# Kernel optimization log

Measured on AMD Instinct MI355X. Metric: run time of the kernel, lower is better.

## Reference

```python
import jax, jax.numpy as jnp
import numpy as np

BLANK = 36
NEG = -1e30  # stand-in for -inf that stays NaN-free under logaddexp


def _ctc_loss(logits, targets, input_lengths, target_lengths):
    """CTC loss (reduction='mean', matching torch.nn.CTCLoss semantics:
    per-sample loss divided by target_length, then mean over batch).
    logits: [B, T, C] raw scores; targets: [B*L] flattened labels (fixed L per sample).
    """
    B, T, C = logits.shape
    L = targets.shape[0] // B
    tgt = targets.reshape(B, L)
    S = 2 * L + 1  # extended label length: blank-interleaved

    # log_softmax over classes, then time-major [T, B, C]
    lp = jnp.transpose(jax.nn.log_softmax(logits, axis=-1), (1, 0, 2))

    # extended targets: [blank, t1, blank, t2, ..., blank]  -> [B, S]
    ext = jnp.full((B, S), BLANK, dtype=tgt.dtype).at[:, 1::2].set(tgt)

    # gather log-probs of extended labels: [T, B, S]
    lp_ext = lp[:, jnp.arange(B)[:, None], ext]

    # positions beyond 2*target_len are invalid
    valid = jnp.arange(S)[None, :] < (2 * target_lengths[:, None] + 1)  # [B, S]
    # skip transition s-2 -> s allowed only if ext[s] != blank and ext[s] != ext[s-2]
    skip_ok = (ext != BLANK) & jnp.concatenate(
        [jnp.zeros((B, 2), bool), ext[:, 2:] != ext[:, :-2]], axis=1)

    end_idx = 2 * target_lengths  # index of final blank; [B]

    def final_ll(alpha):
        e1 = jnp.take_along_axis(alpha, end_idx[:, None], axis=1)[:, 0]
        e2 = jnp.take_along_axis(alpha, (end_idx - 1)[:, None], axis=1)[:, 0]
        return jnp.logaddexp(e1, e2)

    # t = 0 initialization
    alpha0 = jnp.full((B, S), NEG, logits.dtype)
    alpha0 = alpha0.at[:, 0].set(lp_ext[0, :, 0]).at[:, 1].set(lp_ext[0, :, 1])
    alpha0 = jnp.where(valid, alpha0, NEG)
    final0 = jnp.where(input_lengths == 1, final_ll(alpha0), NEG)

    pad1 = jnp.full((B, 1), NEG, logits.dtype)
    pad2 = jnp.full((B, 2), NEG, logits.dtype)

    def step(carry, inp):
        alpha, final = carry
        t, lpe = inp  # lpe: [B, S]
        a1 = jnp.concatenate([pad1, alpha[:, :-1]], axis=1)
        a2 = jnp.where(skip_ok, jnp.concatenate([pad2, alpha[:, :-2]], axis=1), NEG)
        new = jnp.logaddexp(jnp.logaddexp(alpha, a1), a2) + lpe
        new = jnp.where(valid, new, NEG)
        final = jnp.where(input_lengths == t + 1, final_ll(new), final)
        return (new, final), None

    (_, final), _ = jax.lax.scan(step, (alpha0, final0),
                                 (jnp.arange(1, T), lp_ext[1:]))
    return jnp.mean(-final / target_lengths.astype(logits.dtype))


def setup_inputs() -> dict:
    key = jax.random.key(0)
    k1, k2 = jax.random.split(key)
    B, T, C, L = 2048, 256, 37, 16
    logits = jax.random.normal(k1, (B, T, C), dtype=jnp.float32)
    targets = jax.random.randint(k2, (B * L,), 0, 36, dtype=jnp.int32)  # never blank
    input_lengths = jnp.full((B,), T, dtype=jnp.int32)
    target_lengths = jnp.full((B,), L, dtype=jnp.int32)
    return {"logits": logits, "targets": targets,
            "input_lengths": input_lengths, "target_lengths": target_lengths}


def reference(logits, targets, input_lengths, target_lengths):
    return _ctc_loss(logits, targets, input_lengths, target_lengths)
```

## Files before the change

### kernel.cpp

```cpp
#include <hip/hip_runtime.h>

#define BLANK 36
#define NEG -1e30f
#define CC 37

__device__ __forceinline__ float logaddexp_f(float a, float b) {
    float m = fmaxf(a, b);
    float d = fabsf(a - b);
    return m + __logf(1.0f + __expf(-d));
}

__global__ __launch_bounds__(256) void ctc_fused_kernel(
    const float* __restrict__ logits,
    const int*   __restrict__ targets,
    const int*   __restrict__ input_lengths,
    const int*   __restrict__ target_lengths,
    float*       __restrict__ per_sample,
    int B, int T, int L)
{
    __shared__ float lds[4 * 4992];
    const int lane = threadIdx.x & 63;
    const int wib  = threadIdx.x >> 6;
    const int b    = blockIdx.x * 4 + wib;
    if (b >= B) return;

    float* X0 = lds + wib * 4992;
    float* X1 = X0 + 2368;
    float* D0 = X0 + 4736;
    float* D1 = D0 + 64;

    const int S = 2 * L + 1;
    const int tlen = target_lengths[b];
    const int ilen = input_lengths[b];
    const int end_idx = 2 * tlen;

    int ext_s = BLANK;
    if (lane < S && (lane & 1)) ext_s = targets[b * L + (lane >> 1)];
    const int ext_sm2 = __shfl_up(ext_s, 2);
    const bool skip_ok = (lane < S) && (lane >= 2) && (ext_s != BLANK) && (ext_s != ext_sm2);
    const bool valid = lane < (2 * tlen + 1);

    const float4* src = (const float4*)(logits + (size_t)b * T * CC);

    float alpha = NEG, cap = NEG;

    auto STEP = [&](float lpe, int tt) {
        float a1 = __shfl_up(alpha, 1);
        a1 = (lane == 0) ? NEG : a1;
        float a2 = __shfl_up(alpha, 2);
        a2 = skip_ok ? a2 : NEG;
        const float mm = fmaxf(fmaxf(alpha, a1), a2);
        const float ss = __expf(alpha - mm) + __expf(a1 - mm) + __expf(a2 - mm);
        alpha = valid ? (mm + __logf(ss) + lpe) : NEG;
        cap = (ilen == tt + 1) ? alpha : cap;
    };

    {
        float4* dst = (float4*)X0;
        #pragma unroll
        for (int k = 0; k < 9; ++k) dst[k * 64 + lane] = src[k * 64 + lane];
        if (lane < 16) dst[576 + lane] = src[576 + lane];
        __builtin_amdgcn_s_waitcnt(0);
        const float* xr = X0 + lane * CC;
        float m = xr[0];
        #pragma unroll
        for (int c2 = 1; c2 < CC; ++c2) m = fmaxf(m, xr[c2]);
        float ss = 0.0f;
        #pragma unroll
        for (int c2 = 0; c2 < CC; ++c2) ss += __expf(xr[c2] - m);
        D0[lane] = m + __logf(ss);
        __builtin_amdgcn_s_waitcnt(0);
    }

    const int NC = T >> 6;
    for (int c = 0; c < NC; ++c) {
        float* Xb = (c & 1) ? X1 : X0;
        float* Db = (c & 1) ? D1 : D0;
        const bool more = (c + 1 < NC);

        float4 f0 = {}, f1 = {}, f2 = {}, f3 = {}, f4 = {},
               f5 = {}, f6 = {}, f7 = {}, f8 = {}, f9 = {};
        if (more) {
            const float4* s2 = src + (size_t)(c + 1) * 592;
            f0 = s2[lane];       f1 = s2[64 + lane];  f2 = s2[128 + lane];
            f3 = s2[192 + lane]; f4 = s2[256 + lane]; f5 = s2[320 + lane];
            f6 = s2[384 + lane]; f7 = s2[448 + lane]; f8 = s2[512 + lane];
            if (lane < 16) f9 = s2[576 + lane];
        }

        const int tbase = c << 6;
        float p0 = Xb[0 * CC + ext_s] - Db[0];
        float p1 = Xb[1 * CC + ext_s] - Db[1];
        float p2 = Xb[2 * CC + ext_s] - Db[2];
        float p3 = Xb[3 * CC + ext_s] - Db[3];
        float q0, q1, q2, q3;
        int g = 0;
        if (c == 0) {
            alpha = (valid && lane <= 1) ? p0 : NEG;
            cap = (ilen == 1) ? alpha : cap;
            q0 = Xb[4 * CC + ext_s] - Db[4];
            q1 = Xb[5 * CC + ext_s] - Db[5];
            q2 = Xb[6 * CC + ext_s] - Db[6];
            q3 = Xb[7 * CC + ext_s] - Db[7];
            STEP(p1, 1); STEP(p2, 2); STEP(p3, 3);
            p0 = q0; p1 = q1; p2 = q2; p3 = q3;
            g = 1;
        }
        for (; g < 16; ++g) {
            const int r = (g + 1) << 2;
            if (g < 15) {
                q0 = Xb[(r + 0) * CC + ext_s] - Db[r + 0];
                q1 = Xb[(r + 1) * CC + ext_s] - Db[r + 1];
                q2 = Xb[(r + 2) * CC + ext_s] - Db[r + 2];
                q3 = Xb[(r + 3) * CC + ext_s] - Db[r + 3];
            }
            const int tt = tbase + (g << 2);
            STEP(p0, tt); STEP(p1, tt + 1); STEP(p2, tt + 2); STEP(p3, tt + 3);
            p0 = q0; p1 = q1; p2 = q2; p3 = q3;
        }

        if (more) {
            float* Xn = (c & 1) ? X0 : X1;
            float* Dn = (c & 1) ? D0 : D1;
            float4* dst = (float4*)Xn;
            dst[lane] = f0;       dst[64 + lane] = f1;  dst[128 + lane] = f2;
            dst[192 + lane] = f3; dst[256 + lane] = f4; dst[320 + lane] = f5;
            dst[384 + lane] = f6; dst[448 + lane] = f7; dst[512 + lane] = f8;
            if (lane < 16) dst[576 + lane] = f9;
            __builtin_amdgcn_s_waitcnt(0);
            const float* xr = Xn + lane * CC;
            float m = xr[0];
            #pragma unroll
            for (int c2 = 1; c2 < CC; ++c2) m = fmaxf(m, xr[c2]);
            float ss = 0.0f;
            #pragma unroll
            for (int c2 = 0; c2 < CC; ++c2) ss += __expf(xr[c2] - m);
            Dn[lane] = m + __logf(ss);
            __builtin_amdgcn_s_waitcnt(0);
        }
    }

    const float e1 = __shfl(cap, end_idx);
    const float e2 = __shfl(cap, end_idx - 1);
    const float final_v = logaddexp_f(e1, e2);
    if (lane == 0) per_sample[b] = -final_v / (float)tlen;
}

__global__ __launch_bounds__(256) void lse_kernel(
    const float* __restrict__ logits, float* __restrict__ denom, int N)
{
    __shared__ float lds[256 * CC];
    const int lane = threadIdx.x & 63;
    const int wib  = threadIdx.x >> 6;
    const int wave = blockIdx.x * 4 + wib;
    const long long row0 = (long long)wave * 64;
    if (row0 >= N) return;
    const int wbase = wib * 64 * CC;
    const float4* src4 = (const float4*)(logits + row0 * CC);
    const long long n4_remaining = ((long long)N * CC - row0 * CC) / 4;
    float4* lds4 = (float4*)(lds + wbase);
    #pragma unroll
    for (int k = 0; k < 10; ++k) {
        const int idx = k * 64 + lane;
        if (idx < 592 && idx < n4_remaining) lds4[idx] = src4[idx];
    }
    __builtin_amdgcn_s_waitcnt(0);
    const long long row = row0 + lane;
    if (row >= N) return;
    const float* x = lds + wbase + lane * CC;
    float m = x[0];
    #pragma unroll
    for (int c = 1; c < CC; ++c) m = fmaxf(m, x[c]);
    float s = 0.0f;
    #pragma unroll
    for (int c = 0; c < CC; ++c) s += __expf(x[c] - m);
    denom[row] = m + __logf(s);
}

__global__ __launch_bounds__(256) void ctc_alpha2_kernel(
    const float* __restrict__ logits, const float* __restrict__ denom,
    const int* __restrict__ targets, const int* __restrict__ input_lengths,
    const int* __restrict__ target_lengths, float* __restrict__ per_sample,
    int B, int T, int L)
{
    const int wave = (int)((blockIdx.x * blockDim.x + threadIdx.x) >> 6);
    const int lane = threadIdx.x & 63;
    if (wave >= B) return;
    const int b = wave;
    const int S = 2 * L + 1;
    const int tlen = target_lengths[b];
    const int ilen = input_lengths[b];
    const int end_idx = 2 * tlen;
    int ext_s = BLANK;
    if (lane < S && (lane & 1)) ext_s = targets[b * L + (lane >> 1)];
    const int ext_sm2 = __shfl_up(ext_s, 2);
    const bool skip_ok = (lane < S) && (lane >= 2) && (ext_s != BLANK) && (ext_s != ext_sm2);
    const bool valid = lane < (2 * tlen + 1);
    const float* lg = logits + (size_t)b * T * CC;
    const float* dn = denom + (size_t)b * T;
    float x_cur = lg[ext_s];
    float d_cur = dn[0];
    float x_nx = (T > 1) ? lg[CC + ext_s] : 0.0f;
    float d_nx = (T > 1) ? dn[1] : 0.0f;
    float final_v = NEG;
    float alpha = (valid && lane <= 1) ? (x_cur - d_cur) : NEG;
    if (ilen == 1) {
        const float e1 = __shfl(alpha, end_idx);
        const float e2 = __shfl(alpha, end_idx - 1);
        final_v = logaddexp_f(e1, e2);
    }
    for (int tt = 1; tt < T; ++tt) {
        x_cur = x_nx; d_cur = d_nx;
        if (tt + 1 < T) {
            x_nx = lg[(size_t)(tt + 1) * CC + ext_s];
            d_nx = dn[tt + 1];
        }
        const float lpe = x_cur - d_cur;
        float a1 = __shfl_up(alpha, 1);
        if (lane == 0) a1 = NEG;
        float a2 = __shfl_up(alpha, 2);
        if (!skip_ok) a2 = NEG;
        const float m = fmaxf(fmaxf(alpha, a1), a2);
        const float s = __expf(alpha - m) + __expf(a1 - m) + __expf(a2 - m);
        const float na = m + __logf(s) + lpe;
        alpha = valid ? na : NEG;
        if (ilen == tt + 1) {
            const float e1 = __shfl(alpha, end_idx);
            const float e2 = __shfl(alpha, end_idx - 1);
            final_v = logaddexp_f(e1, e2);
        }
    }
    if (lane == 0) per_sample[b] = -final_v / (float)tlen;
}

__global__ __launch_bounds__(256) void ctc_alpha_mono_kernel(
    const float* __restrict__ logits, const int* __restrict__ targets,
    const int* __restrict__ input_lengths, const int* __restrict__ target_lengths,
    float* __restrict__ per_sample, int B, int T, int L)
{
    const int wave = (int)((blockIdx.x * blockDim.x + threadIdx.x) >> 6);
    const int lane = threadIdx.x & 63;
    if (wave >= B) return;
    const int b = wave;
    const int S = 2 * L + 1;
    const int tlen = target_lengths[b];
    const int ilen = input_lengths[b];
    const int end_idx = 2 * tlen;
    int ext_s = BLANK;
    if (lane < S && (lane & 1)) ext_s = targets[b * L + (lane >> 1)];
    const int ext_sm2 = __shfl_up(ext_s, 2);
    const bool skip_ok = (lane < S) && (lane >= 2) && (ext_s != BLANK) && (ext_s != ext_sm2);
    const bool valid = lane < (2 * tlen + 1);
    const float* lg = logits + (size_t)b * T * CC;
    float alpha = NEG, final_v = NEG;
    for (int t = 0; t < T; ++t) {
        float x = (lane < CC) ? lg[t * CC + lane] : -3.0e38f;
        float mx = x;
        #pragma unroll
        for (int o = 32; o > 0; o >>= 1) mx = fmaxf(mx, __shfl_xor(mx, o));
        float e = (lane < CC) ? __expf(x - mx) : 0.0f;
        float se = e;
        #pragma unroll
        for (int o = 32; o > 0; o >>= 1) se += __shfl_xor(se, o);
        const float lp = x - mx - __logf(se);
        const float lpe = __shfl(lp, ext_s);
        float newa;
        if (t == 0) {
            newa = (lane <= 1) ? lpe : NEG;
        } else {
            float a1 = __shfl_up(alpha, 1);
            if (lane == 0) a1 = NEG;
            float a2 = __shfl_up(alpha, 2);
            if (!skip_ok) a2 = NEG;
            newa = logaddexp_f(logaddexp_f(alpha, a1), a2) + lpe;
        }
        if (!valid) newa = NEG;
        alpha = newa;
        if (ilen == t + 1) {
            const float e1 = __shfl(alpha, end_idx);
            const float e2 = __shfl(alpha, end_idx - 1);
            final_v = logaddexp_f(e1, e2);
        }
    }
    if (lane == 0) per_sample[b] = -final_v / (float)tlen;
}

__global__ __launch_bounds__(256) void reduce_mean_kernel(
    const float* __restrict__ ps, float* __restrict__ out, int B)
{
    float s = 0.0f;
    for (int i = threadIdx.x; i < B; i += 256) s += ps[i];
    #pragma unroll
    for (int o = 32; o > 0; o >>= 1) s += __shfl_xor(s, o);
    __shared__ float sm[4];
    const int w = threadIdx.x >> 6, l = threadIdx.x & 63;
    if (l == 0) sm[w] = s;
    __syncthreads();
    if (threadIdx.x == 0) {
        out[0] = (sm[0] + sm[1] + sm[2] + sm[3]) / (float)B;
    }
}

extern "C" void kernel_launch(void* const* d_in, const int* in_sizes, int n_in,
                              void* d_out, int out_size, void* d_ws, size_t ws_size,
                              hipStream_t stream) {
    const float* logits         = (const float*)d_in[0];
    const int*   targets        = (const int*)d_in[1];
    const int*   input_lengths  = (const int*)d_in[2];
    const int*   target_lengths = (const int*)d_in[3];

    const int B = in_sizes[2];
    const int L = in_sizes[1] / B;
    const int T = in_sizes[0] / (B * CC);
    const long long N = (long long)B * T;

    float* per_sample = (float*)d_ws;
    float* scratch    = per_sample + B;
    float* out        = (float*)d_out;

    const size_t ws_mid = ((size_t)B + (size_t)N) * sizeof(float);
    const int nblocks_alpha = (B * 64 + 255) / 256;
    const long long nwaves = (N + 63) / 64;

    if ((T % 64 == 0) && T >= 64 && L <= 31 && ws_size >= (size_t)B * sizeof(float)) {
        ctc_fused_kernel<<<(B + 3) / 4, 256, 0, stream>>>(
            logits, targets, input_lengths, target_lengths, per_sample, B, T, L);
    } else if (ws_size >= ws_mid && T >= 2) {
        lse_kernel<<<(int)((nwaves + 3) / 4), 256, 0, stream>>>(logits, scratch, (int)N);
        ctc_alpha2_kernel<<<nblocks_alpha, 256, 0, stream>>>(
            logits, scratch, targets, input_lengths, target_lengths, per_sample, B, T, L);
    } else {
        ctc_alpha_mono_kernel<<<nblocks_alpha, 256, 0, stream>>>(
            logits, targets, input_lengths, target_lengths, per_sample, B, T, L);
    }
    reduce_mean_kernel<<<1, 256, 0, stream>>>(per_sample, out, B);
}
```

Baseline: 144.7 us.

## Run CTC forward recursion in scaled linear space instead of log space

```diff
diff --git a/kernel.cpp b/kernel.cpp
--- a/kernel.cpp
+++ b/kernel.cpp
@@ -3,6 +3,7 @@
 #define BLANK 36
 #define NEG -1e30f
 #define CC 37
+#define LOG32 3.4657359027997265f
 
 __device__ __forceinline__ float logaddexp_f(float a, float b) {
     float m = fmaxf(a, b);
@@ -10,7 +11,7 @@
     return m + __logf(1.0f + __expf(-d));
 }
 
-__global__ __launch_bounds__(256) void ctc_fused_kernel(
+__global__ __launch_bounds__(256) void ctc_fused_lin_kernel(
     const float* __restrict__ logits,
     const int*   __restrict__ targets,
     const int*   __restrict__ input_lengths,
@@ -18,41 +19,68 @@
     float*       __restrict__ per_sample,
     int B, int T, int L)
 {
-    __shared__ float lds[4 * 4992];
+    __shared__ float lds[4 * 4736];
     const int lane = threadIdx.x & 63;
     const int wib  = threadIdx.x >> 6;
     const int b    = blockIdx.x * 4 + wib;
     if (b >= B) return;
 
-    float* X0 = lds + wib * 4992;
+    float* X0 = lds + wib * 4736;
     float* X1 = X0 + 2368;
-    float* D0 = X0 + 4736;
-    float* D1 = D0 + 64;
 
     const int S = 2 * L + 1;
-    const int tlen = target_lengths[b];
-    const int ilen = input_lengths[b];
-    const int end_idx = 2 * tlen;
+    const int tlen_s = __builtin_amdgcn_readfirstlane(target_lengths[b]);
+    const int ilen_s = __builtin_amdgcn_readfirstlane(input_lengths[b]);
+    const int end_s  = 2 * tlen_s;
 
     int ext_s = BLANK;
     if (lane < S && (lane & 1)) ext_s = targets[b * L + (lane >> 1)];
     const int ext_sm2 = __shfl_up(ext_s, 2);
     const bool skip_ok = (lane < S) && (lane >= 2) && (ext_s != BLANK) && (ext_s != ext_sm2);
-    const bool valid = lane < (2 * tlen + 1);
+    const bool valid = lane < (2 * tlen_s + 1);
 
     const float4* src = (const float4*)(logits + (size_t)b * T * CC);
 
-    float alpha = NEG, cap = NEG;
-
-    auto STEP = [&](float lpe, int tt) {
-        float a1 = __shfl_up(alpha, 1);
-        a1 = (lane == 0) ? NEG : a1;
-        float a2 = __shfl_up(alpha, 2);
-        a2 = skip_ok ? a2 : NEG;
-        const float mm = fmaxf(fmaxf(alpha, a1), a2);
-        const float ss = __expf(alpha - mm) + __expf(a1 - mm) + __expf(a2 - mm);
-        alpha = valid ? (mm + __logf(ss) + lpe) : NEG;
-        cap = (ilen == tt + 1) ? alpha : cap;
+    float z    = 0.0f;
+    float racc = 0.0f;
+    float capv = NEG;
+
+    auto ZSTEP = [&](float p, int tt) {
+        float z1 = __shfl_up(z, 1);
+        z1 = (lane == 0) ? 0.0f : z1;
+        float z2 = __shfl_up(z, 2);
+        z2 = skip_ok ? z2 : 0.0f;
+        const float zn = (z + z1 + z2) * p;
+        z = valid ? zn : 0.0f;
+        if (ilen_s == tt + 1) {
+            capv = __logf(fmaxf(z, 1e-35f)) + racc - (float)(tt + 1) * LOG32;
+        }
+    };
+
+    auto RESCALE = [&]() {
+        float m = z;
+        #pragma unroll
+        for (int o = 32; o > 0; o >>= 1) m = fmaxf(m, __shfl_xor(m, o));
+        m = fmaxf(m, 1e-30f);
+        z *= (1.0f / m);
+        racc += __logf(m);
+    };
+
+    auto SOFTMAX = [&](float* Xn) {
+        float xr[CC];
+        const float* row = Xn + lane * CC;
+        #pragma unroll
+        for (int c2 = 0; c2 < CC; ++c2) xr[c2] = row[c2];
+        float m = xr[0];
+        #pragma unroll
+        for (int c2 = 1; c2 < CC; ++c2) m = fmaxf(m, xr[c2]);
+        float ss = 0.0f;
+        #pragma unroll
+        for (int c2 = 0; c2 < CC; ++c2) { xr[c2] = __expf(xr[c2] - m); ss += xr[c2]; }
+        const float inv = 32.0f / ss;
+        float* wrow = Xn + lane * CC;
+        #pragma unroll
+        for (int c2 = 0; c2 < CC; ++c2) wrow[c2] = xr[c2] * inv;
     };
 
     {
@@ -61,21 +89,13 @@
         for (int k = 0; k < 9; ++k) dst[k * 64 + lane] = src[k * 64 + lane];
         if (lane < 16) dst[576 + lane] = src[576 + lane];
         __builtin_amdgcn_s_waitcnt(0);
-        const float* xr = X0 + lane * CC;
-        float m = xr[0];
-        #pragma unroll
-        for (int c2 = 1; c2 < CC; ++c2) m = fmaxf(m, xr[c2]);
-        float ss = 0.0f;
-        #pragma unroll
-        for (int c2 = 0; c2 < CC; ++c2) ss += __expf(xr[c2] - m);
-        D0[lane] = m + __logf(ss);
+        SOFTMAX(X0);
         __builtin_amdgcn_s_waitcnt(0);
     }
 
     const int NC = T >> 6;
     for (int c = 0; c < NC; ++c) {
         float* Xb = (c & 1) ? X1 : X0;
-        float* Db = (c & 1) ? D1 : D0;
         const bool more = (c + 1 < NC);
 
         float4 f0 = {}, f1 = {}, f2 = {}, f3 = {}, f4 = {},
@@ -89,61 +109,54 @@
         }
 
         const int tbase = c << 6;
-        float p0 = Xb[0 * CC + ext_s] - Db[0];
-        float p1 = Xb[1 * CC + ext_s] - Db[1];
-        float p2 = Xb[2 * CC + ext_s] - Db[2];
-        float p3 = Xb[3 * CC + ext_s] - Db[3];
+        float p0 = Xb[0 * CC + ext_s];
+        float p1 = Xb[1 * CC + ext_s];
+        float p2 = Xb[2 * CC + ext_s];
+        float p3 = Xb[3 * CC + ext_s];
         float q0, q1, q2, q3;
         int g = 0;
         if (c == 0) {
-            alpha = (valid && lane <= 1) ? p0 : NEG;
-            cap = (ilen == 1) ? alpha : cap;
-            q0 = Xb[4 * CC + ext_s] - Db[4];
-            q1 = Xb[5 * CC + ext_s] - Db[5];
-            q2 = Xb[6 * CC + ext_s] - Db[6];
-            q3 = Xb[7 * CC + ext_s] - Db[7];
-            STEP(p1, 1); STEP(p2, 2); STEP(p3, 3);
+            z = (valid && lane <= 1) ? p0 : 0.0f;
+            if (ilen_s == 1) capv = __logf(fmaxf(z, 1e-35f)) - LOG32;
+            q0 = Xb[4 * CC + ext_s];
+            q1 = Xb[5 * CC + ext_s];
+            q2 = Xb[6 * CC + ext_s];
+            q3 = Xb[7 * CC + ext_s];
+            ZSTEP(p1, 1); ZSTEP(p2, 2); ZSTEP(p3, 3);
             p0 = q0; p1 = q1; p2 = q2; p3 = q3;
             g = 1;
         }
         for (; g < 16; ++g) {
             const int r = (g + 1) << 2;
             if (g < 15) {
-                q0 = Xb[(r + 0) * CC + ext_s] - Db[r + 0];
-                q1 = Xb[(r + 1) * CC + ext_s] - Db[r + 1];
-                q2 = Xb[(r + 2) * CC + ext_s] - Db[r + 2];
-                q3 = Xb[(r + 3) * CC + ext_s] - Db[r + 3];
+                q0 = Xb[(r + 0) * CC + ext_s];
+                q1 = Xb[(r + 1) * CC + ext_s];
+                q2 = Xb[(r + 2) * CC + ext_s];
+                q3 = Xb[(r + 3) * CC + ext_s];
             }
             const int tt = tbase + (g << 2);
-            STEP(p0, tt); STEP(p1, tt + 1); STEP(p2, tt + 2); STEP(p3, tt + 3);
+            ZSTEP(p0, tt); ZSTEP(p1, tt + 1); ZSTEP(p2, tt + 2); ZSTEP(p3, tt + 3);
             p0 = q0; p1 = q1; p2 = q2; p3 = q3;
+            if (g & 1) RESCALE();
         }
 
         if (more) {
             float* Xn = (c & 1) ? X0 : X1;
-            float* Dn = (c & 1) ? D0 : D1;
             float4* dst = (float4*)Xn;
             dst[lane] = f0;       dst[64 + lane] = f1;  dst[128 + lane] = f2;
             dst[192 + lane] = f3; dst[256 + lane] = f4; dst[320 + lane] = f5;
             dst[384 + lane] = f6; dst[448 + lane] = f7; dst[512 + lane] = f8;
             if (lane < 16) dst[576 + lane] = f9;
             __builtin_amdgcn_s_waitcnt(0);
-            const float* xr = Xn + lane * CC;
-            float m = xr[0];
-            #pragma unroll
-            for (int c2 = 1; c2 < CC; ++c2) m = fmaxf(m, xr[c2]);
-            float ss = 0.0f;
-            #pragma unroll
-            for (int c2 = 0; c2 < CC; ++c2) ss += __expf(xr[c2] - m);
-            Dn[lane] = m + __logf(ss);
+            SOFTMAX(Xn);
             __builtin_amdgcn_s_waitcnt(0);
         }
     }
 
-    const float e1 = __shfl(cap, end_idx);
-    const float e2 = __shfl(cap, end_idx - 1);
+    const float e1 = __shfl(capv, end_s);
+    const float e2 = __shfl(capv, end_s - 1);
     const float final_v = logaddexp_f(e1, e2);
-    if (lane == 0) per_sample[b] = -final_v / (float)tlen;
+    if (lane == 0) per_sample[b] = -final_v / (float)tlen_s;
 }
 
 __global__ __launch_bounds__(256) void lse_kernel(
@@ -323,7 +336,7 @@
     const long long nwaves = (N + 63) / 64;
 
     if ((T % 64 == 0) && T >= 64 && L <= 31 && ws_size >= (size_t)B * sizeof(float)) {
-        ctc_fused_kernel<<<(B + 3) / 4, 256, 0, stream>>>(
+        ctc_fused_lin_kernel<<<(B + 3) / 4, 256, 0, stream>>>(
             logits, targets, input_lengths, target_lengths, per_sample, B, T, L);
     } else if (ws_size >= ws_mid && T >= 2) {
         lse_kernel<<<(int)((nwaves + 3) / 4), 256, 0, stream>>>(logits, scratch, (int)N);
```

Result: no change. 145.7 us (+0.7%).
